# Optimization experiments

Measured on AMD Instinct MI355X. Metric: run time of the kernel, lower is better.

Reference implementation:

```python
import jax, jax.numpy as jnp
import numpy as np


def _causal_kernel_mask(K):
    # casual_mask[i, K-i:] = 0 for i in 1..p
    p = K // 2
    m = np.ones((p + 1, K), np.float32)
    for i in range(1, p + 1):
        m[i, K - i:] = 0.0
    return jnp.asarray(m)


def setup_inputs() -> dict:
    rng = jax.random.key(0)
    k0, k1, k2, k3, k4 = jax.random.split(rng, 5)
    B, H, N, F = 2, 16, 1024, 64
    V, K = 32000, 5
    return {
        "input_ids": jax.random.randint(k0, (B, N), 0, V),
        "query": jax.random.normal(k1, (B, H, N, F), dtype=jnp.float32),
        "key": jax.random.normal(k2, (B, H, N, F), dtype=jnp.float32),
        "value": jax.random.normal(k3, (B, H, N, F), dtype=jnp.float32),
        "emb_weight": jax.random.normal(k4, (V, 2 * K), dtype=jnp.float32) * 0.02,
    }


def reference(input_ids, query, key, value, emb_weight):
    B, H, N, F = query.shape
    K = emb_weight.shape[1] // 2  # head/layer invariant -> emb dim = 2*K
    p = K // 2
    G = 2 * H

    # ---- get_kernel (layer 0; head_invariant + layer_invariant) ----
    kern = emb_weight[input_ids]                       # [B,N,2K]
    kern = kern.reshape(B, N, 2, 1, K)                 # [B,N,2,1,K]
    kern = jnp.broadcast_to(kern, (B, N, 2, H, K)).reshape(B, N, G, K)

    # ---- conv_key_value (for_casual=True, strict_on_casual=True) ----
    kv = jnp.concatenate([key, value], axis=1)         # [B,2H,N,F]
    kv_pad = jnp.pad(kv, ((0, 0), (0, 0), (p, p), (0, 0)))
    # unfold over token dim: [B,2H,K,N,F]
    kv_unf = jnp.stack([kv_pad[:, :, k:k + N, :] for k in range(K)], axis=2)
    cmask = _causal_kernel_mask(K)                     # [p+1,K]
    kern_m = kern[:, :, :, None, :] * cmask[None, None, None]  # [B,N,2H,p+1,K]
    # dynamic depthwise conv with per-offset causal masking
    out = jnp.einsum('bgknf,bngjk->bgjnf', kv_unf, kern_m)     # [B,2H,p+1,N,F]
    key_c = out[:, :H, 0]                              # [B,H,N,F]
    value_c = out[:, H:, 0]                            # [B,H,N,F]

    # ---- attention with causal-boundary corrections (n_past = 0) ----
    scale = 1.0 / jnp.sqrt(jnp.asarray(F, dtype=query.dtype))
    q = query * scale
    scores = jnp.einsum('bhnf,bhmf->bhnm', q, key_c)   # [B,H,N,N]

    # correct_attn_weights_near_casual_boundary
    for i in range(p):
        off = p - 1 - i
        cb_key = out[:, :H, 1 + i]                     # [B,H,N,F]
        corr = jnp.einsum('bhnf,bhnf->bhn', q[:, :, off:, :], cb_key[:, :, :N - off, :])
        rows = jnp.arange(N - off) + off
        cols = jnp.arange(N - off)
        scores = scores.at[:, :, rows, cols].set(corr)

    causal = jnp.tril(jnp.ones((N, N), dtype=bool))
    scores = jnp.where(causal, scores, jnp.asarray(-1e9, dtype=scores.dtype))
    probs = jax.nn.softmax(scores, axis=-1)
    attn = jnp.einsum('bhnm,bhmf->bhnf', probs, value_c)

    # correct_attn_output_near_casual_boundary
    for i in range(p):
        off = p - 1 - i
        cb_value = out[:, H:, 1 + i]                   # [B,H,N,F]
        idx = jnp.arange(N - off)
        diag_w = probs[:, :, idx + off, idx]           # diag offset=-off: [B,H,N-off]
        diff_v = cb_value[:, :, :N - off, :] - value_c[:, :, :N - off, :]
        diff = diag_w[..., None] * diff_v
        attn = attn + jnp.pad(diff, ((0, 0), (0, 0), (off, 0), (0, 0)))

    return attn
```

## Files before the change

### kernel.cpp

```cpp
#include <hip/hip_runtime.h>

#define HD    64
#define NSEQ  1024
#define LOG2E 1.44269504088896f

typedef __attribute__((ext_vector_type(8))) __bf16 bf16x8;
typedef __attribute__((ext_vector_type(4))) float  f32x4;
typedef __attribute__((ext_vector_type(4))) unsigned short u16x4;

__device__ inline unsigned short f2bf(float x) {
    unsigned u = __float_as_uint(x);
    return (unsigned short)((u + 0x7fffu + ((u >> 16) & 1u)) >> 16);
}
__device__ inline unsigned pk2(float a, float b) {
    return (unsigned)f2bf(a) | ((unsigned)f2bf(b) << 16);
}
__device__ inline float dot4(f32x4 a, f32x4 b) {
    return a.x * b.x + a.y * b.y + a.z * b.z + a.w * b.w;
}

__global__ __launch_bounds__(256) void conv_kernel(
    const int* __restrict__ ids,
    const float* __restrict__ keyg,
    const float* __restrict__ valg,
    const float* __restrict__ qg,
    const float* __restrict__ emb,
    unsigned short* __restrict__ kc,
    unsigned short* __restrict__ vcT,
    float* __restrict__ dg1, float* __restrict__ dg2)
{
    __shared__ __align__(16) float sA[70 * 68];
    __shared__ __align__(16) float sB[70 * 68];
    __shared__ float sE[65 * 10];

    int pid = blockIdx.x;
    int bh = pid & 31;
    int n0 = (pid >> 5) << 6;
    int b  = bh >> 4;
    int t  = threadIdx.x;
    size_t hb = (size_t)bh * NSEQ * HD;
    const float* kb = keyg + hb;
    const float* vb = valg + hb;

    for (int u = t; u < 650; u += 256) {
        int r = u / 10, c = u - r * 10;
        int n = n0 - 1 + r;
        sE[u] = (n >= 0) ? emb[(size_t)ids[b * NSEQ + n] * 10 + c] : 0.f;
    }
    for (int u = t; u < 70 * 16; u += 256) {
        int r = u >> 4, f = (u & 15) << 2;
        int g = n0 - 3 + r;
        f32x4 kv4 = (f32x4){0.f, 0.f, 0.f, 0.f};
        f32x4 vv4 = (f32x4){0.f, 0.f, 0.f, 0.f};
        if (g >= 0 && g < NSEQ) {
            kv4 = *(const f32x4*)(kb + (size_t)g * HD + f);
            vv4 = *(const f32x4*)(vb + (size_t)g * HD + f);
        }
        *(f32x4*)(sA + r * 68 + f) = kv4;
        *(f32x4*)(sB + r * 68 + f) = vv4;
    }
    __syncthreads();

    f32x4 vcv_save[4];
#pragma unroll
    for (int i = 0; i < 4; ++i) {
        int u  = (i << 8) + t;
        int nl = u >> 4, g4 = u & 15;
        int n  = n0 + nl, f = g4 << 2;
        const float* e  = sE + (nl + 1) * 10;
        const float* ep = sE + nl * 10;
        const float* ar = sA + nl * 68 + f;
        const float* br = sB + nl * 68 + f;
        f32x4 km3 = *(const f32x4*)(ar);
        f32x4 x0 = *(const f32x4*)(ar + 68);
        f32x4 x1 = *(const f32x4*)(ar + 2 * 68);
        f32x4 x2 = *(const f32x4*)(ar + 3 * 68);
        f32x4 x3 = *(const f32x4*)(ar + 4 * 68);
        f32x4 x4 = *(const f32x4*)(ar + 5 * 68);
        f32x4 v0 = *(const f32x4*)(br + 68);
        f32x4 v1 = *(const f32x4*)(br + 2 * 68);
        f32x4 v2 = *(const f32x4*)(br + 3 * 68);
        f32x4 v3 = *(const f32x4*)(br + 4 * 68);
        f32x4 v4 = *(const f32x4*)(br + 5 * 68);
        f32x4 qv = *(const f32x4*)(qg + hb + (size_t)n * HD + f) * (0.125f * LOG2E);

        f32x4 k012 = e[0] * x0 + e[1] * x1 + e[2] * x2;
        f32x4 kcv  = k012 + e[3] * x3 + e[4] * x4;
        f32x4 vcv  = e[5] * v0 + e[6] * v1 + e[7] * v2 + e[8] * v3 + e[9] * v4;

        u16x4 kq;
        kq.x = f2bf(kcv.x); kq.y = f2bf(kcv.y); kq.z = f2bf(kcv.z); kq.w = f2bf(kcv.w);
        *(u16x4*)(kc + hb + (size_t)n * HD + f) = kq;
        vcv_save[i] = vcv;

        float s2 = dot4(qv, k012);
        f32x4 kj1 = ep[0] * km3 + ep[1] * x0 + ep[2] * x1 + ep[3] * x2;
        float s1 = dot4(qv, kj1);
#pragma unroll
        for (int o = 1; o < 16; o <<= 1) {
            s2 += __shfl_xor(s2, o, 64);
            s1 += __shfl_xor(s1, o, 64);
        }
        if (g4 == 0) {
            dg2[bh * NSEQ + n] = s2;
            dg1[bh * NSEQ + n] = s1;
        }
    }
    __syncthreads();
    float* vt = sA;
#pragma unroll
    for (int i = 0; i < 4; ++i) {
        int u = (i << 8) + t;
        int nl = u >> 4, f = (u & 15) << 2;
        *(f32x4*)(vt + nl * 68 + f) = vcv_save[i];
    }
    __syncthreads();
#pragma unroll
    for (int i = 0; i < 4; ++i) {
        int u = (i << 8) + t;
        int f = u >> 4, nn = (u & 15) << 2;
        u16x4 o;
        o.x = f2bf(vt[(nn + 0) * 68 + f]);
        o.y = f2bf(vt[(nn + 1) * 68 + f]);
        o.z = f2bf(vt[(nn + 2) * 68 + f]);
        o.w = f2bf(vt[(nn + 3) * 68 + f]);
        *(u16x4*)(vcT + ((size_t)bh * HD + f) * NSEQ + n0 + nn) = o;
    }
}

__global__ __launch_bounds__(512, 4) void attn_kernel(
    const float* __restrict__ qg,
    const unsigned short* __restrict__ kc,
    const unsigned short* __restrict__ vcT,
    const float* __restrict__ dg1, const float* __restrict__ dg2,
    const float* __restrict__ valg, const int* __restrict__ ids,
    const float* __restrict__ emb,
    float* __restrict__ outg)
{
    __shared__ __align__(16) unsigned char sK[2][2][8192];
    __shared__ __align__(16) unsigned char sV[2][2][8192];
    __shared__ __align__(16) unsigned char sP[16384];

    int pid = blockIdx.x;
    int bh  = pid & 31;
    int j   = 15 - (pid >> 5);
    int t   = threadIdx.x;
    int wv  = t >> 6, l = t & 63;
    int grp = wv >> 2;
    int w_in = wv & 3;
    int lq = l & 15, h = l >> 4, l7 = l & 7;
    int qbw = j * 64 + w_in * 16;
    int hA  = (j + 2) >> 1;
    int t0  = grp ? hA : 0;
    int myLen = grp ? (j + 1 - hA) : hA;
    int L   = hA;
    size_t hb = (size_t)bh * NSEQ * HD;

    const unsigned short* kcb = kc  + hb;
    const unsigned short* vtb = vcT + (size_t)bh * HD * NSEQ;

    bf16x8 qb0, qb1;
    {
        const float* qr = qg + hb + (size_t)(qbw + lq) * HD + 8 * h;
        f32x4 a0 = *(const f32x4*)(qr);
        f32x4 a1 = *(const f32x4*)(qr + 4);
        f32x4 b0 = *(const f32x4*)(qr + 32);
        f32x4 b1 = *(const f32x4*)(qr + 36);
        const float S = 0.125f * LOG2E;
        union { unsigned u[4]; bf16x8 v; } u0, u1;
        u0.u[0] = pk2(a0.x * S, a0.y * S); u0.u[1] = pk2(a0.z * S, a0.w * S);
        u0.u[2] = pk2(a1.x * S, a1.y * S); u0.u[3] = pk2(a1.z * S, a1.w * S);
        u1.u[0] = pk2(b0.x * S, b0.y * S); u1.u[1] = pk2(b0.z * S, b0.w * S);
        u1.u[2] = pk2(b1.x * S, b1.y * S); u1.u[3] = pk2(b1.z * S, b1.w * S);
        qb0 = u0.v; qb1 = u1.v;
    }
    float diag2_l = dg2[bh * NSEQ + qbw + lq];
    float diag1_l = dg1[bh * NSEQ + qbw + lq];

    f32x4 of[4];
#pragma unroll
    for (int ft = 0; ft < 4; ++ft) of[ft] = (f32x4){0.f, 0.f, 0.f, 0.f};
    float denom = 0.f;

    const int ka_off0 = ((0 + h) ^ l7) << 4;
    const int ka_off1 = ((4 + h) ^ l7) << 4;
    const int pr_base = wv * 2048 + lq * 128;
    const int chk0 = ((qbw > 0 ? qbw - 1 : 0) >> 6);

    const int tl = t & 255;
    uint4 pf[4];
    auto issue = [&](int tg) {
        int kv0 = tg << 6;
#pragma unroll
        for (int i = 0; i < 4; ++i) {
            int chunk = tl + (i << 8);
            int buf = chunk >> 9, loc = chunk & 511;
            int r = loc >> 3, c = loc & 7;
            int cs = c ^ (r & 7);
            pf[i] = (buf == 0)
                ? *(const uint4*)(kcb + (size_t)(kv0 + r) * HD + cs * 8)
                : *(const uint4*)(vtb + (size_t)r * NSEQ + kv0 + cs * 8);
        }
    };
    auto commit = [&](int cu) {
#pragma unroll
        for (int i = 0; i < 4; ++i) {
            int chunk = tl + (i << 8);
            int buf = chunk >> 9, loc = chunk & 511;
            int r = loc >> 3, c = loc & 7;
            *(uint4*)((buf ? sV[grp][cu] : sK[grp][cu]) + r * 128 + c * 16) = pf[i];
        }
    };

    if (myLen > 0) { issue(t0); commit(0); }
    if (myLen > 1) issue(t0 + 1);
    __syncthreads();

    for (int ti = 0; ti < L; ++ti) {
        int cur = ti & 1;
        if (ti + 1 < myLen) commit(cur ^ 1);
        if (ti + 2 < myLen) issue(t0 + ti + 2);
        int tg  = t0 + ti;
        int kv0 = tg << 6;
        bool act = (ti < myLen);

        if (act) {
            const unsigned char* sKc = sK[grp][cur];
            const unsigned char* sVc = sV[grp][cur];
            f32x4 p[4];
            __builtin_amdgcn_s_setprio(1);
#pragma unroll
            for (int st = 0; st < 4; ++st) {
                bf16x8 ka0 = *(const bf16x8*)(sKc + st * 2048 + lq * 128 + ka_off0);
                bf16x8 ka1 = *(const bf16x8*)(sKc + st * 2048 + lq * 128 + ka_off1);
                f32x4 d = (f32x4){0.f, 0.f, 0.f, 0.f};
                d = __builtin_amdgcn_mfma_f32_16x16x32_bf16(ka0, qb0, d, 0, 0, 0);
                d = __builtin_amdgcn_mfma_f32_16x16x32_bf16(ka1, qb1, d, 0, 0, 0);
                p[st] = d;
            }
            __builtin_amdgcn_s_setprio(0);

            if (tg >= chk0) {
                int n_l = qbw + lq;
#pragma unroll
                for (int st = 0; st < 4; ++st)
#pragma unroll
                    for (int r = 0; r < 4; ++r) {
                        int kv = kv0 + st * 16 + 4 * h + r;
                        float dd = p[st][r];
                        if (kv > n_l)           dd = -1e30f;
                        else if (kv == n_l)     dd = diag2_l;
                        else if (kv == n_l - 1) dd = diag1_l;
                        p[st][r] = dd;
                    }
            }

            float lsum = 0.f;
#pragma unroll
            for (int st = 0; st < 4; ++st)
#pragma unroll
                for (int r = 0; r < 4; ++r) {
                    float e = __builtin_exp2f(p[st][r]);
                    p[st][r] = e;
                    lsum += e;
                }
            lsum += __shfl_xor(lsum, 16, 64);
            lsum += __shfl_xor(lsum, 32, 64);
            denom += lsum;

#pragma unroll
            for (int st = 0; st < 4; ++st) {
                uint2 uu;
                uu.x = pk2(p[st][0], p[st][1]);
                uu.y = pk2(p[st][2], p[st][3]);
                int chunk = (st << 1) + (h >> 1);
                *(uint2*)(sP + pr_base + ((chunk ^ l7) << 4) + ((h & 1) << 3)) = uu;
            }
            asm volatile("s_waitcnt lgkmcnt(0)" ::: "memory");
            __builtin_amdgcn_sched_barrier(0);

            __builtin_amdgcn_s_setprio(1);
#pragma unroll
            for (int kk = 0; kk < 2; ++kk) {
                int koff = kk ? ka_off1 : ka_off0;
                bf16x8 pa = *(const bf16x8*)(sP + pr_base + koff);
#pragma unroll
                for (int ft = 0; ft < 4; ++ft) {
                    bf16x8 vb = *(const bf16x8*)(sVc + ft * 2048 + lq * 128 + koff);
                    of[ft] = __builtin_amdgcn_mfma_f32_16x16x32_bf16(pa, vb, of[ft], 0, 0, 0);
                }
            }
            __builtin_amdgcn_s_setprio(0);
        }
        if (ti + 1 < L) __syncthreads();
    }

    __syncthreads();
    float* mrg = (float*)sK;
    if (grp == 1) {
        float* d = mrg + (size_t)tl * 17;
#pragma unroll
        for (int ft = 0; ft < 4; ++ft) {
            d[4 * ft + 0] = of[ft].x;
            d[4 * ft + 1] = of[ft].y;
            d[4 * ft + 2] = of[ft].z;
            d[4 * ft + 3] = of[ft].w;
        }
        d[16] = denom;
    }
    __syncthreads();
    if (grp == 1) return;

    {
        const float* s = mrg + (size_t)tl * 17;
#pragma unroll
        for (int ft = 0; ft < 4; ++ft) {
            of[ft].x += s[4 * ft + 0];
            of[ft].y += s[4 * ft + 1];
            of[ft].z += s[4 * ft + 2];
            of[ft].w += s[4 * ft + 3];
        }
        denom += s[16];
    }

    const float* vraw = valg + hb;
    float* outr = outg + hb;
    const int* idb = ids + (size_t)(bh >> 4) * NSEQ;
#pragma unroll
    for (int r = 0; r < 4; ++r) {
        int qrow = 4 * h + r;
        int n = qbw + qrow;
        float dn = __shfl(denom,   qrow, 64);
        float d2 = __shfl(diag2_l, qrow, 64);
        float d1 = __shfl(diag1_l, qrow, 64);
        float inv = 1.0f / dn;
        float p2 = __builtin_exp2f(d2) * inv;
        float p1 = (n >= 1) ? __builtin_exp2f(d1) * inv : 0.f;
        int id_n = idb[n];
        float e8  = emb[(size_t)id_n * 10 + 8];
        float e9  = emb[(size_t)id_n * 10 + 9];
        float e9p = (n >= 1) ? emb[(size_t)idb[n - 1] * 10 + 9] : 0.f;
        float ca = -(p2 * e8 + p1 * e9p);
        float cb = -p2 * e9;
#pragma unroll
        for (int ft = 0; ft < 4; ++ft) {
            int f = ft * 16 + lq;
            float v = of[ft][r] * inv;
            if (n + 1 < NSEQ) v += ca * vraw[(size_t)(n + 1) * HD + f];
            if (n + 2 < NSEQ) v += cb * vraw[(size_t)(n + 2) * HD + f];
            outr[(size_t)n * HD + f] = v;
        }
    }
}

extern "C" void kernel_launch(void* const* d_in, const int* in_sizes, int n_in,
                              void* d_out, int out_size, void* d_ws, size_t ws_size,
                              hipStream_t stream)
{
    const int*   ids = (const int*)  d_in[0];
    const float* q   = (const float*)d_in[1];
    const float* key = (const float*)d_in[2];
    const float* val = (const float*)d_in[3];
    const float* emb = (const float*)d_in[4];
    float* out = (float*)d_out;

    char* w = (char*)d_ws;
    unsigned short* kc  = (unsigned short*)(w);
    unsigned short* vcT = (unsigned short*)(w + (4u << 20));
    float* dg1 = (float*)(w + 8388608);
    float* dg2 = (float*)(w + 8519680);

    conv_kernel<<<512, 256, 0, stream>>>(ids, key, val, q, emb, kc, vcT, dg1, dg2);
    attn_kernel<<<512, 512, 0, stream>>>(q, kc, vcT, dg1, dg2, val, ids, emb, out);
}
```

Measured before the change: 54.37 us.

## Drop split-KV wave groups in attention kernel, use single 256-thread block

Removes the two-group split of the KV range inside each attention block, in which each half processed half the key tiles and the partial outputs were then merged through shared memory. Each 256-thread block now walks all key tiles serially, so the LDS footprint drops and the merge step and extra synchronisation go away. The cost is less parallelism per query tile and a longer serial loop for the late causal tiles, which may hurt load balance and latency hiding.

New measurement: 60.06 us. 1.1x slower.

```diff
diff --git a/kernel.cpp b/kernel.cpp
--- a/kernel.cpp
+++ b/kernel.cpp
@@ -128,7 +128,7 @@
     }
 }
 
-__global__ __launch_bounds__(512, 4) void attn_kernel(
+__global__ __launch_bounds__(256, 4) void attn_kernel(
     const float* __restrict__ qg,
     const unsigned short* __restrict__ kc,
     const unsigned short* __restrict__ vcT,
@@ -137,23 +137,19 @@
     const float* __restrict__ emb,
     float* __restrict__ outg)
 {
-    __shared__ __align__(16) unsigned char sK[2][2][8192];
-    __shared__ __align__(16) unsigned char sV[2][2][8192];
-    __shared__ __align__(16) unsigned char sP[16384];
+    __shared__ __align__(16) unsigned char sK[2][8192];
+    __shared__ __align__(16) unsigned char sV[2][8192];
+    __shared__ __align__(16) unsigned char sP[8192];
 
     int pid = blockIdx.x;
     int bh  = pid & 31;
     int j   = 15 - (pid >> 5);
-    int t   = threadIdx.x;
-    int wv  = t >> 6, l = t & 63;
-    int grp = wv >> 2;
-    int w_in = wv & 3;
+    int len = j + 1;
+
+    int t = threadIdx.x;
+    int w = t >> 6, l = t & 63;
     int lq = l & 15, h = l >> 4, l7 = l & 7;
-    int qbw = j * 64 + w_in * 16;
-    int hA  = (j + 2) >> 1;
-    int t0  = grp ? hA : 0;
-    int myLen = grp ? (j + 1 - hA) : hA;
-    int L   = hA;
+    int qbw = j * 64 + w * 16;
     size_t hb = (size_t)bh * NSEQ * HD;
 
     const unsigned short* kcb = kc  + hb;
@@ -184,16 +180,15 @@
 
     const int ka_off0 = ((0 + h) ^ l7) << 4;
     const int ka_off1 = ((4 + h) ^ l7) << 4;
-    const int pr_base = wv * 2048 + lq * 128;
+    const int pr_base = w * 2048 + lq * 128;
     const int chk0 = ((qbw > 0 ? qbw - 1 : 0) >> 6);
 
-    const int tl = t & 255;
     uint4 pf[4];
     auto issue = [&](int tg) {
         int kv0 = tg << 6;
 #pragma unroll
         for (int i = 0; i < 4; ++i) {
-            int chunk = tl + (i << 8);
+            int chunk = t + (i << 8);
             int buf = chunk >> 9, loc = chunk & 511;
             int r = loc >> 3, c = loc & 7;
             int cs = c ^ (r & 7);
@@ -205,122 +200,90 @@
     auto commit = [&](int cu) {
 #pragma unroll
         for (int i = 0; i < 4; ++i) {
-            int chunk = tl + (i << 8);
+            int chunk = t + (i << 8);
             int buf = chunk >> 9, loc = chunk & 511;
             int r = loc >> 3, c = loc & 7;
-            *(uint4*)((buf ? sV[grp][cu] : sK[grp][cu]) + r * 128 + c * 16) = pf[i];
+            *(uint4*)((buf ? sV[cu] : sK[cu]) + r * 128 + c * 16) = pf[i];
         }
     };
 
-    if (myLen > 0) { issue(t0); commit(0); }
-    if (myLen > 1) issue(t0 + 1);
+    issue(0); commit(0);
+    if (len > 1) issue(1);
     __syncthreads();
 
-    for (int ti = 0; ti < L; ++ti) {
+    for (int ti = 0; ti < len; ++ti) {
         int cur = ti & 1;
-        if (ti + 1 < myLen) commit(cur ^ 1);
-        if (ti + 2 < myLen) issue(t0 + ti + 2);
-        int tg  = t0 + ti;
-        int kv0 = tg << 6;
-        bool act = (ti < myLen);
-
-        if (act) {
-            const unsigned char* sKc = sK[grp][cur];
-            const unsigned char* sVc = sV[grp][cur];
-            f32x4 p[4];
-            __builtin_amdgcn_s_setprio(1);
-#pragma unroll
-            for (int st = 0; st < 4; ++st) {
-                bf16x8 ka0 = *(const bf16x8*)(sKc + st * 2048 + lq * 128 + ka_off0);
-                bf16x8 ka1 = *(const bf16x8*)(sKc + st * 2048 + lq * 128 + ka_off1);
-                f32x4 d = (f32x4){0.f, 0.f, 0.f, 0.f};
-                d = __builtin_amdgcn_mfma_f32_16x16x32_bf16(ka0, qb0, d, 0, 0, 0);
-                d = __builtin_amdgcn_mfma_f32_16x16x32_bf16(ka1, qb1, d, 0, 0, 0);
-                p[st] = d;
+        if (ti + 1 < len) commit(cur ^ 1);
+        if (ti + 2 < len) issue(ti + 2);
+        int kv0 = ti << 6;
+        const unsigned char* sKc = sK[cur];
+        const unsigned char* sVc = sV[cur];
+
+        f32x4 p[4];
+        __builtin_amdgcn_s_setprio(1);
+#pragma unroll
+        for (int st = 0; st < 4; ++st) {
+            bf16x8 ka0 = *(const bf16x8*)(sKc + st * 2048 + lq * 128 + ka_off0);
+            bf16x8 ka1 = *(const bf16x8*)(sKc + st * 2048 + lq * 128 + ka_off1);
+            f32x4 d = (f32x4){0.f, 0.f, 0.f, 0.f};
+            d = __builtin_amdgcn_mfma_f32_16x16x32_bf16(ka0, qb0, d, 0, 0, 0);
+            d = __builtin_amdgcn_mfma_f32_16x16x32_bf16(ka1, qb1, d, 0, 0, 0);
+            p[st] = d;
+        }
+        __builtin_amdgcn_s_setprio(0);
+
+        if (ti >= chk0) {
+            int n_l = qbw + lq;
+#pragma unroll
+            for (int st = 0; st < 4; ++st)
+#pragma unroll
+                for (int r = 0; r < 4; ++r) {
+                    int kv = kv0 + st * 16 + 4 * h + r;
+                    float dd = p[st][r];
+                    if (kv > n_l)           dd = -1e30f;
+                    else if (kv == n_l)     dd = diag2_l;
+                    else if (kv == n_l - 1) dd = diag1_l;
+                    p[st][r] = dd;
+                }
+        }
+
+        float lsum = 0.f;
+#pragma unroll
+        for (int st = 0; st < 4; ++st)
+#pragma unroll
+            for (int r = 0; r < 4; ++r) {
+                float e = __builtin_exp2f(p[st][r]);
+                p[st][r] = e;
+                lsum += e;
             }
-            __builtin_amdgcn_s_setprio(0);
-
-            if (tg >= chk0) {
-                int n_l = qbw + lq;
-#pragma unroll
-                for (int st = 0; st < 4; ++st)
-#pragma unroll
-                    for (int r = 0; r < 4; ++r) {
-                        int kv = kv0 + st * 16 + 4 * h + r;
-                        float dd = p[st][r];
-                        if (kv > n_l)           dd = -1e30f;
-                        else if (kv == n_l)     dd = diag2_l;
-                        else if (kv == n_l - 1) dd = diag1_l;
-                        p[st][r] = dd;
-                    }
+        lsum += __shfl_xor(lsum, 16, 64);
+        lsum += __shfl_xor(lsum, 32, 64);
+        denom += lsum;
+
+#pragma unroll
+        for (int st = 0; st < 4; ++st) {
+            uint2 uu;
+            uu.x = pk2(p[st][0], p[st][1]);
+            uu.y = pk2(p[st][2], p[st][3]);
+            int chunk = (st << 1) + (h >> 1);
+            *(uint2*)(sP + pr_base + ((chunk ^ l7) << 4) + ((h & 1) << 3)) = uu;
+        }
+        asm volatile("s_waitcnt lgkmcnt(0)" ::: "memory");
+        __builtin_amdgcn_sched_barrier(0);
+
+        __builtin_amdgcn_s_setprio(1);
+#pragma unroll
+        for (int kk = 0; kk < 2; ++kk) {
+            int koff = kk ? ka_off1 : ka_off0;
+            bf16x8 pa = *(const bf16x8*)(sP + pr_base + koff);
+#pragma unroll
+            for (int ft = 0; ft < 4; ++ft) {
+                bf16x8 vb = *(const bf16x8*)(sVc + ft * 2048 + lq * 128 + koff);
+                of[ft] = __builtin_amdgcn_mfma_f32_16x16x32_bf16(pa, vb, of[ft], 0, 0, 0);
             }
-
-            float lsum = 0.f;
-#pragma unroll
-            for (int st = 0; st < 4; ++st)
-#pragma unroll
-                for (int r = 0; r < 4; ++r) {
-                    float e = __builtin_exp2f(p[st][r]);
-                    p[st][r] = e;
-                    lsum += e;
-                }
-            lsum += __shfl_xor(lsum, 16, 64);
-            lsum += __shfl_xor(lsum, 32, 64);
-            denom += lsum;
-
-#pragma unroll
-            for (int st = 0; st < 4; ++st) {
-                uint2 uu;
-                uu.x = pk2(p[st][0], p[st][1]);
-                uu.y = pk2(p[st][2], p[st][3]);
-                int chunk = (st << 1) + (h >> 1);
-                *(uint2*)(sP + pr_base + ((chunk ^ l7) << 4) + ((h & 1) << 3)) = uu;
-            }
-            asm volatile("s_waitcnt lgkmcnt(0)" ::: "memory");
-            __builtin_amdgcn_sched_barrier(0);
-
-            __builtin_amdgcn_s_setprio(1);
-#pragma unroll
-            for (int kk = 0; kk < 2; ++kk) {
-                int koff = kk ? ka_off1 : ka_off0;
-                bf16x8 pa = *(const bf16x8*)(sP + pr_base + koff);
-#pragma unroll
-                for (int ft = 0; ft < 4; ++ft) {
-                    bf16x8 vb = *(const bf16x8*)(sVc + ft * 2048 + lq * 128 + koff);
-                    of[ft] = __builtin_amdgcn_mfma_f32_16x16x32_bf16(pa, vb, of[ft], 0, 0, 0);
-                }
-            }
-            __builtin_amdgcn_s_setprio(0);
-        }
-        if (ti + 1 < L) __syncthreads();
-    }
-
-    __syncthreads();
-    float* mrg = (float*)sK;
-    if (grp == 1) {
-        float* d = mrg + (size_t)tl * 17;
-#pragma unroll
-        for (int ft = 0; ft < 4; ++ft) {
-            d[4 * ft + 0] = of[ft].x;
-            d[4 * ft + 1] = of[ft].y;
-            d[4 * ft + 2] = of[ft].z;
-            d[4 * ft + 3] = of[ft].w;
-        }
-        d[16] = denom;
-    }
-    __syncthreads();
-    if (grp == 1) return;
-
-    {
-        const float* s = mrg + (size_t)tl * 17;
-#pragma unroll
-        for (int ft = 0; ft < 4; ++ft) {
-            of[ft].x += s[4 * ft + 0];
-            of[ft].y += s[4 * ft + 1];
-            of[ft].z += s[4 * ft + 2];
-            of[ft].w += s[4 * ft + 3];
-        }
-        denom += s[16];
+        }
+        __builtin_amdgcn_s_setprio(0);
+        if (ti + 1 < len) __syncthreads();
     }
 
     const float* vraw = valg + hb;
@@ -371,5 +334,5 @@
     float* dg2 = (float*)(w + 8519680);
 
     conv_kernel<<<512, 256, 0, stream>>>(ids, key, val, q, emb, kc, vcT, dg1, dg2);
-    attn_kernel<<<512, 512, 0, stream>>>(q, kc, vcT, dg1, dg2, val, ids, emb, out);
-}
+    attn_kernel<<<512, 256, 0, stream>>>(q, kc, vcT, dg1, dg2, val, ids, emb, out);
+}
```
